# Performance work log

Hardware: AMD Instinct MI355X
Metric: run time of the kernel (lower is better)

Reference implementation:

```python
import jax, jax.numpy as jnp
import numpy as np

B, D, H, N, M, K = 128, 256, 4, 256, 256, 10  # M=256 is hardcoded in the original repeat(1,1,1,256)
DIM = D // H  # per-head dim = 64


def setup_inputs() -> dict:
    key = jax.random.key(0)
    ks = jax.random.split(key, 10)
    s = 0.05  # weight scale
    return {
        "x": jax.random.normal(ks[0], (B, D, N), jnp.float32),
        "source": jax.random.normal(ks[1], (B, D, M), jnp.float32),
        "Wq": jax.random.normal(ks[2], (D, D), jnp.float32) * s,
        "bq": jax.random.normal(ks[3], (D,), jnp.float32) * s,
        "Wk": jax.random.normal(ks[4], (D, D), jnp.float32) * s,
        "bk": jax.random.normal(ks[5], (D,), jnp.float32) * s,
        "Wv": jax.random.normal(ks[6], (D, D), jnp.float32) * s,
        "bv": jax.random.normal(ks[7], (D,), jnp.float32) * s,
        "Wm": jax.random.normal(ks[8], (D, D), jnp.float32) * s,
        "bm": jax.random.normal(ks[9], (D,), jnp.float32) * s,
        "k": K,
    }


def _pointwise(W, b, x):
    # nn.Conv1d(d, d, kernel_size=1): per-point linear over channel dim
    return jnp.einsum('ef,bfn->ben', W, x) + b[None, :, None]


def reference(x, source, Wq, bq, Wk, bk, Wv, bv, Wm, bm, k):
    b, d, n = x.shape
    # torch .view(b, dim, heads, -1) splits channels as (dim, heads)
    q = _pointwise(Wq, bq, x).reshape(b, DIM, H, n)
    kk = _pointwise(Wk, bk, source).reshape(b, DIM, H, -1)
    v = _pointwise(Wv, bv, source).reshape(b, DIM, H, -1)

    scores = jnp.einsum('bdhn,bdhm->bhnm', q, kk) / jnp.sqrt(jnp.asarray(DIM, x.dtype))
    # per-row top-k threshold: keep only scores >= k-th largest, softmax over kept
    thresh = jax.lax.top_k(scores, k)[0][..., k - 1:k]  # [b,h,n,1]
    mask = scores >= thresh
    neg = jnp.finfo(scores.dtype).min
    prob = jax.nn.softmax(jnp.where(mask, scores, neg), axis=-1)
    prob = jnp.where(mask, prob, jnp.zeros((), scores.dtype))

    out = jnp.einsum('bhnm,bdhm->bdhn', prob, v).reshape(b, d, n)
    return _pointwise(Wm, bm, out)
```

## Files before the change

### kernel.cpp

```cpp
#include <hip/hip_runtime.h>
#include <hip/hip_bf16.h>

#define BB   128
#define DDIM 256
#define HH   4
#define NNN  256
#define MMM  256

typedef __hip_bfloat16 bf16;
typedef short  short8   __attribute__((ext_vector_type(8)));
typedef unsigned short ushort8_t __attribute__((ext_vector_type(8)));
typedef float  f32x4    __attribute__((ext_vector_type(4)));

__device__ __forceinline__ unsigned short f2bf(float x) {
    unsigned u = __builtin_bit_cast(unsigned, x);
    u += 0x7FFFu + ((u >> 16) & 1u);
    return (unsigned short)(u >> 16);
}
__device__ __forceinline__ float bf2f(unsigned short b) {
    unsigned u = ((unsigned)b) << 16;
    return __builtin_bit_cast(float, u);
}

__device__ __forceinline__ void xpose4(float v[4], const int p) {
    float ta = __shfl_xor((p & 1) ? v[0] : v[1], 1, 64);
    float tb = __shfl_xor((p & 1) ? v[2] : v[3], 1, 64);
    float u0 = (p & 1) ? ta : v[0];
    float u1 = (p & 1) ? v[1] : ta;
    float u2 = (p & 1) ? tb : v[2];
    float u3 = (p & 1) ? v[3] : tb;
    float tc = __shfl_xor((p & 2) ? u0 : u2, 2, 64);
    float td = __shfl_xor((p & 2) ? u1 : u3, 2, 64);
    v[0] = (p & 2) ? tc : u0;
    v[1] = (p & 2) ? td : u1;
    v[2] = (p & 2) ? u2 : tc;
    v[3] = (p & 2) ? u3 : td;
}

__device__ __forceinline__ void split3_store8k(char* dst, const float v[4]) {
    unsigned short h[4], m[4], l[4];
    #pragma unroll
    for (int i = 0; i < 4; ++i) {
        h[i] = f2bf(v[i]);
        float r1 = v[i] - bf2f(h[i]);
        m[i] = f2bf(r1);
        float r2 = r1 - bf2f(m[i]);
        l[i] = f2bf(r2);
    }
    uint2 hp, mp, lp;
    hp.x = (unsigned)h[0] | ((unsigned)h[1] << 16);
    hp.y = (unsigned)h[2] | ((unsigned)h[3] << 16);
    mp.x = (unsigned)m[0] | ((unsigned)m[1] << 16);
    mp.y = (unsigned)m[2] | ((unsigned)m[3] << 16);
    lp.x = (unsigned)l[0] | ((unsigned)l[1] << 16);
    lp.y = (unsigned)l[2] | ((unsigned)l[3] << 16);
    *(uint2*)dst = hp;
    *(uint2*)(dst + 8192) = mp;
    *(uint2*)(dst + 16384) = lp;
}

__device__ __forceinline__ void split2_store(char* dst, const float v[4]) {
    unsigned short h[4], m[4];
    #pragma unroll
    for (int i = 0; i < 4; ++i) {
        h[i] = f2bf(v[i]);
        float r1 = v[i] - bf2f(h[i]);
        m[i] = f2bf(r1);
    }
    uint2 hp, mp;
    hp.x = (unsigned)h[0] | ((unsigned)h[1] << 16);
    hp.y = (unsigned)h[2] | ((unsigned)h[3] << 16);
    mp.x = (unsigned)m[0] | ((unsigned)m[1] << 16);
    mp.y = (unsigned)m[2] | ((unsigned)m[3] << 16);
    *(uint2*)dst = hp;
    *(uint2*)(dst + 16384) = mp;
}

__device__ __forceinline__ void ldx4(const float* p, float v[4]) {
    const float4 f = *(const float4*)p;
    v[0] = f.x; v[1] = f.y; v[2] = f.z; v[3] = f.w;
}
__device__ __forceinline__ void ldx4(const bf16* p, float v[4]) {
    uint2 u = *(const uint2*)p;
    v[0] = bf2f((unsigned short)(u.x & 0xFFFF));
    v[1] = bf2f((unsigned short)(u.x >> 16));
    v[2] = bf2f((unsigned short)(u.y & 0xFFFF));
    v[3] = bf2f((unsigned short)(u.y >> 16));
}

__device__ __forceinline__ float max16v(const float* w) {
    float a = fmaxf(fmaxf(w[0], w[1]),  fmaxf(w[2], w[3]));
    float b = fmaxf(fmaxf(w[4], w[5]),  fmaxf(w[6], w[7]));
    float c = fmaxf(fmaxf(w[8], w[9]),  fmaxf(w[10], w[11]));
    float d = fmaxf(fmaxf(w[12], w[13]), fmaxf(w[14], w[15]));
    return fmaxf(fmaxf(a, b), fmaxf(c, d));
}
__device__ __forceinline__ float gmax16(float v) {
    v = fmaxf(v, __shfl_xor(v, 1, 64));
    v = fmaxf(v, __shfl_xor(v, 2, 64));
    v = fmaxf(v, __shfl_xor(v, 4, 64));
    v = fmaxf(v, __shfl_xor(v, 8, 64));
    return v;
}
__device__ __forceinline__ float gsum16(float v) {
    v += __shfl_xor(v, 1, 64);
    v += __shfl_xor(v, 2, 64);
    v += __shfl_xor(v, 4, 64);
    v += __shfl_xor(v, 8, 64);
    return v;
}

__global__ __launch_bounds__(256)
void proj_kernel(const float* __restrict__ X, const float* __restrict__ W,
                 const float* __restrict__ bias, float* __restrict__ Y) {
    __shared__ float Wt[32][68];
    __shared__ float Xt[32][132];

    const int t  = threadIdx.x;
    const int tx = t & 31;
    const int ty = t >> 5;
    const int n0 = blockIdx.x * 128;
    const int e0 = blockIdx.y * 64;
    const int b  = blockIdx.z;
    const size_t plane = (size_t)b * DDIM * NNN;

    float acc[8][4] = {};

    for (int f0 = 0; f0 < DDIM; f0 += 32) {
        #pragma unroll
        for (int i = 0; i < 8; ++i) {
            int idx = t + i * 256;
            int fl = idx & 31, el = idx >> 5;
            Wt[fl][el] = W[(size_t)(e0 + el) * DDIM + f0 + fl];
        }
        #pragma unroll
        for (int i = 0; i < 4; ++i) {
            int idx = t + i * 256;
            int fl = idx >> 5, nl4 = idx & 31;
            *(float4*)&Xt[fl][nl4 * 4] =
                *(const float4*)&X[plane + (size_t)(f0 + fl) * NNN + n0 + nl4 * 4];
        }
        __syncthreads();

        #pragma unroll
        for (int ff = 0; ff < 32; ++ff) {
            const float4 av0 = *(const float4*)&Wt[ff][ty * 8];
            const float4 av1 = *(const float4*)&Wt[ff][ty * 8 + 4];
            const float4 bv  = *(const float4*)&Xt[ff][tx * 4];
            const float a[8] = {av0.x, av0.y, av0.z, av0.w, av1.x, av1.y, av1.z, av1.w};
            const float c[4] = {bv.x, bv.y, bv.z, bv.w};
            #pragma unroll
            for (int i2 = 0; i2 < 8; ++i2)
                #pragma unroll
                for (int j = 0; j < 4; ++j)
                    acc[i2][j] = fmaf(a[i2], c[j], acc[i2][j]);
        }
        __syncthreads();
    }

    #pragma unroll
    for (int i2 = 0; i2 < 8; ++i2) {
        const int e = e0 + ty * 8 + i2;
        const float bs = bias[e];
        const size_t off = plane + (size_t)e * NNN + n0 + tx * 4;
        float4 o;
        o.x = acc[i2][0] + bs; o.y = acc[i2][1] + bs;
        o.z = acc[i2][2] + bs; o.w = acc[i2][3] + bs;
        *(float4*)&Y[off] = o;
    }
}

template <typename TIN, typename TOUT>
__global__ __launch_bounds__(512, 2)
void projm_kernel(const TIN* __restrict__ X, const float* __restrict__ W,
                  const float* __restrict__ bias, TOUT* __restrict__ Y) {
    extern __shared__ __align__(16) char smem[];

    const int t    = threadIdx.x;
    const int lane = t & 63;
    const int w    = t >> 6;
    const int c16  = lane & 15;
    const int g    = (lane >> 4) & 3;
    const int p    = lane & 3;
    const int G    = lane >> 2;

    const int n0 = blockIdx.x * 128;
    const int e0 = blockIdx.y * 128;
    const int b  = blockIdx.z;
    const size_t plane = (size_t)b * DDIM * NNN;

    f32x4 acc[8];
    #pragma unroll
    for (int nf = 0; nf < 8; ++nf) acc[nf] = f32x4{0.f, 0.f, 0.f, 0.f};

    #pragma unroll
    for (int ft = 0; ft < 4; ++ft) {
        const int f0 = ft * 64;
        if (ft) __syncthreads();
        #pragma unroll
        for (int it = 0; it < 4; ++it) {
            int chunk = w + 8 * it;
            int fch = chunk & 15, nh = chunk >> 4;
            float v[4];
            ldx4(&X[plane + (size_t)(f0 + fch * 4 + p) * NNN + n0 + nh * 64 + G * 4], v);
            xpose4(v, p);
            int nl = nh * 64 + G * 4 + p;
            int base = nl * 128 + ((fch * 8) ^ ((nl & 7) << 4));
            split2_store(smem + base, v);
        }
        #pragma unroll
        for (int it = 0; it < 4; ++it) {
            int idx = t + 512 * it;
            int el = idx >> 4, fq = idx & 15;
            float v[4];
            const float4 f4 = *(const float4*)&W[(size_t)(e0 + el) * DDIM + f0 + fq * 4];
            v[0] = f4.x; v[1] = f4.y; v[2] = f4.z; v[3] = f4.w;
            int base = 32768 + el * 128 + ((fq * 8) ^ ((el & 7) << 4));
            split2_store(smem + base, v);
        }
        __syncthreads();

        const int ew = w * 16;
        short8 a0[2], a1[2];
        #pragma unroll
        for (int ks = 0; ks < 2; ++ks) {
            int off = 32768 + (ew + c16) * 128
                    + ((ks * 64 + g * 16) ^ ((c16 & 7) << 4));
            a0[ks] = *(const short8*)(smem + off);
            a1[ks] = *(const short8*)(smem + off + 16384);
        }
        #pragma unroll
        for (int nf = 0; nf < 8; ++nf) {
            #pragma unroll
            for (int ks = 0; ks < 2; ++ks) {
                int off = (nf * 16 + c16) * 128
                        + ((ks * 64 + g * 16) ^ ((c16 & 7) << 4));
                short8 b0 = *(const short8*)(smem + off);
                short8 b1 = *(const short8*)(smem + off + 16384);
                f32x4 a = acc[nf];
                a = __builtin_amdgcn_mfma_f32_16x16x32_bf16(a0[ks], b0, a, 0, 0, 0);
                a = __builtin_amdgcn_mfma_f32_16x16x32_bf16(a0[ks], b1, a, 0, 0, 0);
                a = __builtin_amdgcn_mfma_f32_16x16x32_bf16(a1[ks], b0, a, 0, 0, 0);
                acc[nf] = a;
            }
        }
    }

    const int ew = w * 16;
    float bs[4];
    #pragma unroll
    for (int r = 0; r < 4; ++r) bs[r] = bias[e0 + ew + g * 4 + r];
    #pragma unroll
    for (int nf = 0; nf < 8; ++nf) {
        #pragma unroll
        for (int r = 0; r < 4; ++r) {
            size_t off = plane + (size_t)(e0 + ew + g * 4 + r) * NNN + n0 + nf * 16 + c16;
            float val = acc[nf][r] + bs[r];
            if constexpr (sizeof(TOUT) == 4) Y[off] = val;
            else                             *(unsigned short*)&Y[off] = f2bf(val);
        }
    }
}

__global__ __launch_bounds__(256, 3)
void attn3_kernel(const float* __restrict__ qf, const float* __restrict__ kf,
                  const bf16* __restrict__ vb, bf16* __restrict__ ob,
                  const int* __restrict__ kptr) {
    extern __shared__ __align__(16) char smem[];

    const int t    = threadIdx.x;
    const int lane = t & 63;
    const int w    = t >> 6;
    const int g    = lane >> 4;
    const int c16  = lane & 15;

    const int i    = blockIdx.x;
    const int work = (i & 7) * 256 + (i >> 3);
    const int bx = work & 3;
    const int h  = (work >> 2) & 3;
    const int b  = work >> 4;
    const int n0 = bx * 64;

    const size_t planeF = (size_t)b * DDIM * NNN;
    const size_t planeV = (size_t)b * DDIM * MMM;

    int kk = kptr[0];
    kk = kk < 1 ? 1 : (kk > MMM ? MMM : kk);

    {
        const int p = lane & 3, G = lane >> 2;
        #pragma unroll
        for (int it = 0; it < 4; ++it) {
            int dch = w + 4 * it;
            int drow = dch * 4 + p;
            float v[4];
            const float4 f4 = *(const float4*)&qf[planeF + (size_t)(drow * HH + h) * NNN + n0 + G * 4];
            v[0] = f4.x * 0.125f; v[1] = f4.y * 0.125f;
            v[2] = f4.z * 0.125f; v[3] = f4.w * 0.125f;
            xpose4(v, p);
            int nl = G * 4 + p;
            int base = nl * 128 + ((dch * 8) ^ ((nl & 7) << 4));
            split3_store8k(smem + base, v);
        }
    }
    __syncthreads();

    short8 qh[2], qm[2], ql[2];
    #pragma unroll
    for (int ks = 0; ks < 2; ++ks) {
        int nl = w * 16 + c16;
        int off = nl * 128 + ((ks * 64 + g * 16) ^ ((nl & 7) << 4));
        qh[ks] = *(const short8*)(smem + off);
        qm[ks] = *(const short8*)(smem + 8192 + off);
        ql[ks] = *(const short8*)(smem + 16384 + off);
    }

    f32x4 acc[16];
    #pragma unroll
    for (int m = 0; m < 16; ++m) acc[m] = f32x4{0.f, 0.f, 0.f, 0.f};

    #pragma unroll
    for (int tt = 0; tt < 4; ++tt) {
        if (tt) __syncthreads();
        {
            const int p = lane & 3, G = lane >> 2;
            #pragma unroll
            for (int it = 0; it < 4; ++it) {
                int dch = w + 4 * it;
                int drow = dch * 4 + p;
                int mcol = tt * 64 + G * 4;
                float v[4];
                const float4 f4 = *(const float4*)&kf[planeF + (size_t)(drow * HH + h) * MMM + mcol];
                v[0] = f4.x; v[1] = f4.y; v[2] = f4.z; v[3] = f4.w;
                xpose4(v, p);
                int ml = G * 4 + p;
                int base = 24576 + ml * 128 + ((dch * 8) ^ ((ml & 7) << 4));
                split3_store8k(smem + base, v);
            }
        }
        __syncthreads();
        #pragma unroll
        for (int mf = 0; mf < 4; ++mf) {
            #pragma unroll
            for (int ks = 0; ks < 2; ++ks) {
                int ml = mf * 16 + c16;
                int off = 24576 + ml * 128 + ((ks * 64 + g * 16) ^ ((ml & 7) << 4));
                short8 bh = *(const short8*)(smem + off);
                short8 bm = *(const short8*)(smem + 8192 + off);
                short8 bl = *(const short8*)(smem + 16384 + off);
                f32x4 a = acc[tt * 4 + mf];
                a = __builtin_amdgcn_mfma_f32_16x16x32_bf16(qh[ks], bh, a, 0, 0, 0);
                a = __builtin_amdgcn_mfma_f32_16x16x32_bf16(qh[ks], bm, a, 0, 0, 0);
                a = __builtin_amdgcn_mfma_f32_16x16x32_bf16(qm[ks], bh, a, 0, 0, 0);
                a = __builtin_amdgcn_mfma_f32_16x16x32_bf16(qm[ks], bm, a, 0, 0, 0);
                a = __builtin_amdgcn_mfma_f32_16x16x32_bf16(qh[ks], bl, a, 0, 0, 0);
                a = __builtin_amdgcn_mfma_f32_16x16x32_bf16(ql[ks], bh, a, 0, 0, 0);
                acc[tt * 4 + mf] = a;
            }
        }
    }
    __syncthreads();

    float thr[4], rmx[4];
    #pragma unroll
    for (int r = 0; r < 4; ++r) {
        float w16[16];
        #pragma unroll
        for (int mf = 0; mf < 16; ++mf) w16[mf] = acc[mf][r];
        float lm = max16v(w16);
        float gm = gmax16(lm);
        rmx[r] = gm;
        for (int it = 1; it < kk; ++it) {
            unsigned long long bal = __ballot(lm == gm);
            unsigned gmask = (unsigned)((bal >> (g * 16)) & 0xFFFFull);
            int leader = __builtin_ctz(gmask);
            bool skip = (c16 != leader);
            #pragma unroll
            for (int mf = 0; mf < 16; ++mf) {
                bool hit = (!skip) && (w16[mf] == gm);
                w16[mf] = hit ? -INFINITY : w16[mf];
                skip = skip || hit;
            }
            lm = max16v(w16);
            gm = gmax16(lm);
        }
        thr[r] = gm;
    }

    #pragma unroll
    for (int mf = 0; mf < 16; ++mf) {
        #pragma unroll
        for (int r = 0; r < 4; ++r) {
            float a = acc[mf][r];
            acc[mf][r] = (a >= thr[r]) ? __expf(a - rmx[r]) : 0.f;
        }
    }
    float inv_[4];
    #pragma unroll
    for (int r = 0; r < 4; ++r) {
        float s = ((acc[0][r] + acc[1][r]) + (acc[2][r] + acc[3][r]))
                + ((acc[4][r] + acc[5][r]) + (acc[6][r] + acc[7][r]))
                + ((acc[8][r] + acc[9][r]) + (acc[10][r] + acc[11][r]))
                + ((acc[12][r] + acc[13][r]) + (acc[14][r] + acc[15][r]));
        s = gsum16(s);
        inv_[r] = 1.0f / s;
    }
    #pragma unroll
    for (int mf = 0; mf < 16; ++mf) {
        #pragma unroll
        for (int r = 0; r < 4; ++r) {
            int row = w * 16 + g * 4 + r;
            int m2  = (mf * 16 + c16) * 2;
            int off = row * 512 + (m2 ^ ((row & 7) << 4));
            *(unsigned short*)(smem + off) = f2bf(acc[mf][r] * inv_[r]);
        }
    }

    f32x4 o[4];
    #pragma unroll
    for (int df = 0; df < 4; ++df) o[df] = f32x4{0.f, 0.f, 0.f, 0.f};

    #pragma unroll
    for (int half = 0; half < 2; ++half) {
        if (half) __syncthreads();
        #pragma unroll
        for (int it = 0; it < 4; ++it) {
            int idx = t + it * 256;
            int d = idx >> 4, mc8 = idx & 15;
            ushort8_t val = *(const ushort8_t*)
                &vb[planeV + (size_t)(d * HH + h) * MMM + half * 128 + mc8 * 8];
            int off = 32768 + d * 256 + ((mc8 * 16) ^ ((d & 7) << 4));
            *(ushort8_t*)(smem + off) = val;
        }
        __syncthreads();

        short8 pa[4];
        #pragma unroll
        for (int ks = 0; ks < 4; ++ks) {
            int row = w * 16 + c16;
            int off = row * 512 + ((half * 256 + ks * 64 + g * 16) ^ ((row & 7) << 4));
            pa[ks] = *(const short8*)(smem + off);
        }
        #pragma unroll
        for (int df = 0; df < 4; ++df) {
            int d = df * 16 + c16;
            f32x4 o_ = o[df];
            #pragma unroll
            for (int ks = 0; ks < 4; ++ks) {
                int off = 32768 + d * 256 + ((ks * 64 + g * 16) ^ ((d & 7) << 4));
                short8 vv = *(const short8*)(smem + off);
                o_ = __builtin_amdgcn_mfma_f32_16x16x32_bf16(pa[ks], vv, o_, 0, 0, 0);
            }
            o[df] = o_;
        }
    }
    __syncthreads();

    #pragma unroll
    for (int df = 0; df < 4; ++df)
        #pragma unroll
        for (int r = 0; r < 4; ++r) {
            int d  = df * 16 + c16;
            int nl = w * 16 + g * 4 + r;
            int off = d * 128 + ((nl * 2) ^ ((d & 7) << 4));
            *(unsigned short*)(smem + off) = f2bf(o[df][r]);
        }
    __syncthreads();
    #pragma unroll
    for (int it = 0; it < 2; ++it) {
        int idx = t + it * 256;
        int d = idx >> 3, ch = idx & 7;
        int off = d * 128 + ((ch * 16) ^ ((d & 7) << 4));
        ushort8_t val = *(const ushort8_t*)(smem + off);
        *(ushort8_t*)&ob[planeV + (size_t)(d * HH + h) * NNN + n0 + ch * 8] = val;
    }
}

extern "C" void kernel_launch(void* const* d_in, const int* in_sizes, int n_in,
                              void* d_out, int out_size, void* d_ws, size_t ws_size,
                              hipStream_t stream) {
    const float* x   = (const float*)d_in[0];
    const float* src = (const float*)d_in[1];
    const float* Wq  = (const float*)d_in[2];
    const float* bq  = (const float*)d_in[3];
    const float* Wk  = (const float*)d_in[4];
    const float* bk  = (const float*)d_in[5];
    const float* Wv  = (const float*)d_in[6];
    const float* bv  = (const float*)d_in[7];
    const float* Wm  = (const float*)d_in[8];
    const float* bm  = (const float*)d_in[9];
    const int*   kp  = (const int*)d_in[10];
    float* out = (float*)d_out;

    const size_t F32PLANE  = (size_t)BB * DDIM * NNN * sizeof(float);
    const size_t BF16PLANE = F32PLANE / 2;
    char* ws = (char*)d_ws;
    float* qf = (float*)(ws);
    float* kf = (float*)(ws + F32PLANE);
    bf16*  vb = (bf16*)(ws + 2 * F32PLANE);
    bf16*  ob = (bf16*)(ws + 2 * F32PLANE + BF16PLANE);

    hipFuncSetAttribute((const void*)(projm_kernel<float, bf16>),
                        hipFuncAttributeMaxDynamicSharedMemorySize, 65536);
    hipFuncSetAttribute((const void*)(projm_kernel<bf16, float>),
                        hipFuncAttributeMaxDynamicSharedMemorySize, 65536);
    hipFuncSetAttribute((const void*)attn3_kernel,
                        hipFuncAttributeMaxDynamicSharedMemorySize, 49152);

    dim3 fgrid(NNN / 128, DDIM / 64, BB);
    hipLaunchKernelGGL(proj_kernel, fgrid, dim3(256), 0, stream, x,   Wq, bq, qf);
    hipLaunchKernelGGL(proj_kernel, fgrid, dim3(256), 0, stream, src, Wk, bk, kf);

    dim3 mgrid(2, 2, BB);
    hipLaunchKernelGGL((projm_kernel<float, bf16>), mgrid, dim3(512), 65536, stream,
                       src, Wv, bv, vb);

    hipLaunchKernelGGL(attn3_kernel, dim3(2048), dim3(256), 49152, stream,
                       qf, kf, vb, ob, kp);

    hipLaunchKernelGGL((projm_kernel<bf16, float>), mgrid, dim3(512), 65536, stream,
                       ob, Wm, bm, out);
}
```

Before: 280.4 us.

## Pre-split K into bf16 triple planes and transpose Q/K layout for attention

The Q/K projection kernel now writes outputs in a per-head transposed [b,h,n,d] layout, and K is emitted as three bf16 planes (high/mid/low split) instead of fp32. A new attention kernel loads those pre-split K planes directly into LDS with global_load_lds, which removes the per-block fp32-to-bf16x3 splitting of K and cuts LDS usage so four blocks can run per CU. The projection inner loop is also rewritten with packed two-wide FMAs. The change falls back to the old path when the workspace is too small, and the scattered 2-byte stores in the projection epilogue may cost write bandwidth.

```diff
diff --git a/kernel.cpp b/kernel.cpp
--- a/kernel.cpp
+++ b/kernel.cpp
@@ -11,6 +11,7 @@
 typedef short  short8   __attribute__((ext_vector_type(8)));
 typedef unsigned short ushort8_t __attribute__((ext_vector_type(8)));
 typedef float  f32x4    __attribute__((ext_vector_type(4)));
+typedef float  f32x2    __attribute__((ext_vector_type(2)));
 
 __device__ __forceinline__ unsigned short f2bf(float x) {
     unsigned u = __builtin_bit_cast(unsigned, x);
@@ -110,9 +111,13 @@
     return v;
 }
 
+
+template <int MODE>
 __global__ __launch_bounds__(256)
-void proj_kernel(const float* __restrict__ X, const float* __restrict__ W,
-                 const float* __restrict__ bias, float* __restrict__ Y) {
+void projqk_kernel(const float* __restrict__ X, const float* __restrict__ W,
+                   const float* __restrict__ bias, float* __restrict__ Yt,
+                   unsigned short* __restrict__ Ph, unsigned short* __restrict__ Pm,
+                   unsigned short* __restrict__ Pl) {
     __shared__ float Wt[32][68];
     __shared__ float Xt[32][132];
 
@@ -124,7 +129,12 @@
     const int b  = blockIdx.z;
     const size_t plane = (size_t)b * DDIM * NNN;
 
-    float acc[8][4] = {};
+    f32x2 acc2[8][2];
+    #pragma unroll
+    for (int i = 0; i < 8; ++i) {
+        acc2[i][0] = f32x2{0.f, 0.f};
+        acc2[i][1] = f32x2{0.f, 0.f};
+    }
 
     for (int f0 = 0; f0 < DDIM; f0 += 32) {
         #pragma unroll
@@ -148,12 +158,14 @@
             const float4 av1 = *(const float4*)&Wt[ff][ty * 8 + 4];
             const float4 bv  = *(const float4*)&Xt[ff][tx * 4];
             const float a[8] = {av0.x, av0.y, av0.z, av0.w, av1.x, av1.y, av1.z, av1.w};
-            const float c[4] = {bv.x, bv.y, bv.z, bv.w};
-            #pragma unroll
-            for (int i2 = 0; i2 < 8; ++i2)
-                #pragma unroll
-                for (int j = 0; j < 4; ++j)
-                    acc[i2][j] = fmaf(a[i2], c[j], acc[i2][j]);
+            const f32x2 c0 = {bv.x, bv.y};
+            const f32x2 c1 = {bv.z, bv.w};
+            #pragma unroll
+            for (int i2 = 0; i2 < 8; ++i2) {
+                const f32x2 aa = {a[i2], a[i2]};
+                acc2[i2][0] = __builtin_elementwise_fma(aa, c0, acc2[i2][0]);
+                acc2[i2][1] = __builtin_elementwise_fma(aa, c1, acc2[i2][1]);
+            }
         }
         __syncthreads();
     }
@@ -161,12 +173,225 @@
     #pragma unroll
     for (int i2 = 0; i2 < 8; ++i2) {
         const int e = e0 + ty * 8 + i2;
+        const int hh = e & 3, dd = e >> 2;
         const float bs = bias[e];
-        const size_t off = plane + (size_t)e * NNN + n0 + tx * 4;
-        float4 o;
-        o.x = acc[i2][0] + bs; o.y = acc[i2][1] + bs;
-        o.z = acc[i2][2] + bs; o.w = acc[i2][3] + bs;
-        *(float4*)&Y[off] = o;
+        const float vals[4] = {acc2[i2][0].x + bs, acc2[i2][0].y + bs,
+                               acc2[i2][1].x + bs, acc2[i2][1].y + bs};
+        #pragma unroll
+        for (int j = 0; j < 4; ++j) {
+            const size_t off = ((size_t)(b * 4 + hh) * NNN + n0 + tx * 4 + j) * 64 + dd;
+            if constexpr (MODE == 0) {
+                Yt[off] = vals[j];
+            } else {
+                unsigned short hv = f2bf(vals[j]);
+                float r1 = vals[j] - bf2f(hv);
+                unsigned short mv = f2bf(r1);
+                float r2 = r1 - bf2f(mv);
+                unsigned short lv = f2bf(r2);
+                Ph[off] = hv; Pm[off] = mv; Pl[off] = lv;
+            }
+        }
+    }
+}
+
+__global__ __launch_bounds__(256, 4)
+void attn4_kernel(const float* __restrict__ qt,
+                  const unsigned short* __restrict__ khp,
+                  const unsigned short* __restrict__ kmp,
+                  const unsigned short* __restrict__ klp,
+                  const bf16* __restrict__ vb, bf16* __restrict__ ob,
+                  const int* __restrict__ kptr) {
+    extern __shared__ __align__(16) char smem[];
+
+    const int t    = threadIdx.x;
+    const int lane = t & 63;
+    const int w    = t >> 6;
+    const int g    = lane >> 4;
+    const int c16  = lane & 15;
+
+    const int i    = blockIdx.x;
+    const int work = (i & 7) * 256 + (i >> 3);
+    const int bx = work & 3;
+    const int h  = (work >> 2) & 3;
+    const int b  = work >> 4;
+    const int n0 = bx * 64;
+    const int bh = b * 4 + h;
+
+    const size_t planeV = (size_t)b * DDIM * MMM;
+
+    int kk = kptr[0];
+    kk = kk < 1 ? 1 : (kk > MMM ? MMM : kk);
+
+    #pragma unroll
+    for (int it = 0; it < 4; ++it) {
+        int gid = t + it * 256;
+        int dq = gid & 15;
+        int n  = gid >> 4;
+        const float4 q4 = *(const float4*)&qt[((size_t)bh * NNN + n0 + n) * 64 + dq * 4];
+        float v[4] = {q4.x * 0.125f, q4.y * 0.125f, q4.z * 0.125f, q4.w * 0.125f};
+        int base = n * 128 + ((dq * 8) ^ ((n & 7) << 4));
+        split3_store8k(smem + base, v);
+    }
+    __syncthreads();
+
+    short8 qh[2], qm[2], ql[2];
+    #pragma unroll
+    for (int ks = 0; ks < 2; ++ks) {
+        int nl = w * 16 + c16;
+        int off = nl * 128 + ((ks * 64 + g * 16) ^ ((nl & 7) << 4));
+        qh[ks] = *(const short8*)(smem + off);
+        qm[ks] = *(const short8*)(smem + 8192 + off);
+        ql[ks] = *(const short8*)(smem + 16384 + off);
+    }
+    __syncthreads();
+
+    f32x4 acc[16];
+    #pragma unroll
+    for (int m = 0; m < 16; ++m) acc[m] = f32x4{0.f, 0.f, 0.f, 0.f};
+
+    #pragma unroll
+    for (int tt = 0; tt < 4; ++tt) {
+        if (tt) __syncthreads();
+        #pragma unroll
+        for (int it = 0; it < 6; ++it) {
+            int gid = t + it * 256;
+            int pl  = gid >> 9;
+            int rem = gid & 511;
+            int ml  = rem >> 3;
+            int dq  = rem & 7;
+            int dqs = dq ^ (ml & 7);
+            const unsigned short* kp = (pl == 0) ? khp : (pl == 1 ? kmp : klp);
+            const unsigned short* src = kp + ((size_t)bh * MMM + tt * 64 + ml) * 64 + dqs * 8;
+            __builtin_amdgcn_global_load_lds(
+                (const __attribute__((address_space(1))) void*)src,
+                (__attribute__((address_space(3))) void*)(smem + gid * 16),
+                16, 0, 0);
+        }
+        __syncthreads();
+
+        #pragma unroll
+        for (int mf = 0; mf < 4; ++mf) {
+            #pragma unroll
+            for (int ks = 0; ks < 2; ++ks) {
+                int ml = mf * 16 + c16;
+                int off = ml * 128 + ((ks * 64 + g * 16) ^ ((ml & 7) << 4));
+                short8 bh_ = *(const short8*)(smem + off);
+                short8 bm_ = *(const short8*)(smem + 8192 + off);
+                short8 bl_ = *(const short8*)(smem + 16384 + off);
+                f32x4 a = acc[tt * 4 + mf];
+                a = __builtin_amdgcn_mfma_f32_16x16x32_bf16(qh[ks], bh_, a, 0, 0, 0);
+                a = __builtin_amdgcn_mfma_f32_16x16x32_bf16(qh[ks], bm_, a, 0, 0, 0);
+                a = __builtin_amdgcn_mfma_f32_16x16x32_bf16(qm[ks], bh_, a, 0, 0, 0);
+                a = __builtin_amdgcn_mfma_f32_16x16x32_bf16(qm[ks], bm_, a, 0, 0, 0);
+                a = __builtin_amdgcn_mfma_f32_16x16x32_bf16(qh[ks], bl_, a, 0, 0, 0);
+                a = __builtin_amdgcn_mfma_f32_16x16x32_bf16(ql[ks], bh_, a, 0, 0, 0);
+                acc[tt * 4 + mf] = a;
+            }
+        }
+    }
+    __syncthreads();
+
+    float thr[4], rmx[4];
+    #pragma unroll
+    for (int r = 0; r < 4; ++r) {
+        float w16[16];
+        #pragma unroll
+        for (int mf = 0; mf < 16; ++mf) w16[mf] = acc[mf][r];
+        float lm = max16v(w16);
+        float gm = gmax16(lm);
+        rmx[r] = gm;
+        for (int it = 1; it < kk; ++it) {
+            unsigned long long bal = __ballot(lm == gm);
+            unsigned gmask = (unsigned)((bal >> (g * 16)) & 0xFFFFull);
+            int leader = __builtin_ctz(gmask);
+            bool skip = (c16 != leader);
+            #pragma unroll
+            for (int mf = 0; mf < 16; ++mf) {
+                bool hit = (!skip) && (w16[mf] == gm);
+                w16[mf] = hit ? -INFINITY : w16[mf];
+                skip = skip || hit;
+            }
+            lm = max16v(w16);
+            gm = gmax16(lm);
+        }
+        thr[r] = gm;
+    }
+
+    #pragma unroll
+    for (int mf = 0; mf < 16; ++mf) {
+        #pragma unroll
+        for (int r = 0; r < 4; ++r) {
+            float a = acc[mf][r];
+            acc[mf][r] = (a >= thr[r]) ? __expf(a - rmx[r]) : 0.f;
+        }
+    }
+    float inv_[4];
+    #pragma unroll
+    for (int r = 0; r < 4; ++r) {
+        float s = ((acc[0][r] + acc[1][r]) + (acc[2][r] + acc[3][r]))
+                + ((acc[4][r] + acc[5][r]) + (acc[6][r] + acc[7][r]))
+                + ((acc[8][r] + acc[9][r]) + (acc[10][r] + acc[11][r]))
+                + ((acc[12][r] + acc[13][r]) + (acc[14][r] + acc[15][r]));
+        s = gsum16(s);
+        inv_[r] = 1.0f / s;
+    }
+    #pragma unroll
+    for (int mf = 0; mf < 16; ++mf) {
+        #pragma unroll
+        for (int r = 0; r < 4; ++r) {
+            int row = w * 16 + g * 4 + r;
+            int m2  = (mf * 16 + c16) * 2;
+            int off = row * 512 + (m2 ^ ((row & 7) << 4));
+            *(unsigned short*)(smem + off) = f2bf(acc[mf][r] * inv_[r]);
+        }
+    }
+    __syncthreads();
+
+    f32x4 o[4];
+    #pragma unroll
+    for (int df = 0; df < 4; ++df) o[df] = f32x4{0.f, 0.f, 0.f, 0.f};
+
+    #pragma unroll
+    for (int half = 0; half < 2; ++half) {
+        short8 pa[4];
+        #pragma unroll
+        for (int ks = 0; ks < 4; ++ks) {
+            int row = w * 16 + c16;
+            int off = row * 512 + ((half * 256 + ks * 64 + g * 16) ^ ((row & 7) << 4));
+            pa[ks] = *(const short8*)(smem + off);
+        }
+        #pragma unroll
+        for (int df = 0; df < 4; ++df) {
+            int d = df * 16 + c16;
+            const bf16* vrow = vb + planeV + (size_t)(d * HH + h) * MMM + half * 128;
+            f32x4 o_ = o[df];
+            #pragma unroll
+            for (int ks = 0; ks < 4; ++ks) {
+                short8 vv = *(const short8*)(vrow + ks * 32 + g * 8);
+                o_ = __builtin_amdgcn_mfma_f32_16x16x32_bf16(pa[ks], vv, o_, 0, 0, 0);
+            }
+            o[df] = o_;
+        }
+    }
+    __syncthreads();
+
+    #pragma unroll
+    for (int df = 0; df < 4; ++df)
+        #pragma unroll
+        for (int r = 0; r < 4; ++r) {
+            int d  = df * 16 + c16;
+            int nl = w * 16 + g * 4 + r;
+            int off = d * 128 + ((nl * 2) ^ ((d & 7) << 4));
+            *(unsigned short*)(smem + off) = f2bf(o[df][r]);
+        }
+    __syncthreads();
+    #pragma unroll
+    for (int it = 0; it < 2; ++it) {
+        int idx = t + it * 256;
+        int d = idx >> 3, ch = idx & 7;
+        int off = d * 128 + ((ch * 16) ^ ((d & 7) << 4));
+        ushort8_t val = *(const ushort8_t*)(smem + off);
+        *(ushort8_t*)&ob[planeV + (size_t)(d * HH + h) * NNN + n0 + ch * 8] = val;
     }
 }
 
@@ -259,6 +484,66 @@
             if constexpr (sizeof(TOUT) == 4) Y[off] = val;
             else                             *(unsigned short*)&Y[off] = f2bf(val);
         }
+    }
+}
+
+__global__ __launch_bounds__(256)
+void proj_kernel(const float* __restrict__ X, const float* __restrict__ W,
+                 const float* __restrict__ bias, float* __restrict__ Y) {
+    __shared__ float Wt[32][68];
+    __shared__ float Xt[32][132];
+
+    const int t  = threadIdx.x;
+    const int tx = t & 31;
+    const int ty = t >> 5;
+    const int n0 = blockIdx.x * 128;
+    const int e0 = blockIdx.y * 64;
+    const int b  = blockIdx.z;
+    const size_t plane = (size_t)b * DDIM * NNN;
+
+    float acc[8][4] = {};
+
+    for (int f0 = 0; f0 < DDIM; f0 += 32) {
+        #pragma unroll
+        for (int i = 0; i < 8; ++i) {
+            int idx = t + i * 256;
+            int fl = idx & 31, el = idx >> 5;
+            Wt[fl][el] = W[(size_t)(e0 + el) * DDIM + f0 + fl];
+        }
+        #pragma unroll
+        for (int i = 0; i < 4; ++i) {
+            int idx = t + i * 256;
+            int fl = idx >> 5, nl4 = idx & 31;
+            *(float4*)&Xt[fl][nl4 * 4] =
+                *(const float4*)&X[plane + (size_t)(f0 + fl) * NNN + n0 + nl4 * 4];
+        }
+        __syncthreads();
+
+        #pragma unroll
+        for (int ff = 0; ff < 32; ++ff) {
+            const float4 av0 = *(const float4*)&Wt[ff][ty * 8];
+            const float4 av1 = *(const float4*)&Wt[ff][ty * 8 + 4];
+            const float4 bv  = *(const float4*)&Xt[ff][tx * 4];
+            const float a[8] = {av0.x, av0.y, av0.z, av0.w, av1.x, av1.y, av1.z, av1.w};
+            const float c[4] = {bv.x, bv.y, bv.z, bv.w};
+            #pragma unroll
+            for (int i2 = 0; i2 < 8; ++i2)
+                #pragma unroll
+                for (int j = 0; j < 4; ++j)
+                    acc[i2][j] = fmaf(a[i2], c[j], acc[i2][j]);
+        }
+        __syncthreads();
+    }
+
+    #pragma unroll
+    for (int i2 = 0; i2 < 8; ++i2) {
+        const int e = e0 + ty * 8 + i2;
+        const float bs = bias[e];
+        const size_t off = plane + (size_t)e * NNN + n0 + tx * 4;
+        float4 o;
+        o.x = acc[i2][0] + bs; o.y = acc[i2][1] + bs;
+        o.z = acc[i2][2] + bs; o.w = acc[i2][3] + bs;
+        *(float4*)&Y[off] = o;
     }
 }
 
@@ -492,32 +777,57 @@
     const int*   kp  = (const int*)d_in[10];
     float* out = (float*)d_out;
 
-    const size_t F32PLANE  = (size_t)BB * DDIM * NNN * sizeof(float);
-    const size_t BF16PLANE = F32PLANE / 2;
     char* ws = (char*)d_ws;
-    float* qf = (float*)(ws);
-    float* kf = (float*)(ws + F32PLANE);
-    bf16*  vb = (bf16*)(ws + 2 * F32PLANE);
-    bf16*  ob = (bf16*)(ws + 2 * F32PLANE + BF16PLANE);
+    const size_t QT_BYTES = 33554432;
+    const size_t PL_BYTES = 16777216;
+    const size_t FAST_NEED = QT_BYTES + 3 * PL_BYTES + 2 * PL_BYTES;
 
     hipFuncSetAttribute((const void*)(projm_kernel<float, bf16>),
                         hipFuncAttributeMaxDynamicSharedMemorySize, 65536);
     hipFuncSetAttribute((const void*)(projm_kernel<bf16, float>),
                         hipFuncAttributeMaxDynamicSharedMemorySize, 65536);
-    hipFuncSetAttribute((const void*)attn3_kernel,
-                        hipFuncAttributeMaxDynamicSharedMemorySize, 49152);
-
-    dim3 fgrid(NNN / 128, DDIM / 64, BB);
-    hipLaunchKernelGGL(proj_kernel, fgrid, dim3(256), 0, stream, x,   Wq, bq, qf);
-    hipLaunchKernelGGL(proj_kernel, fgrid, dim3(256), 0, stream, src, Wk, bk, kf);
-
+
+    dim3 pqk_grid(NNN / 128, DDIM / 64, BB);
     dim3 mgrid(2, 2, BB);
-    hipLaunchKernelGGL((projm_kernel<float, bf16>), mgrid, dim3(512), 65536, stream,
-                       src, Wv, bv, vb);
-
-    hipLaunchKernelGGL(attn3_kernel, dim3(2048), dim3(256), 49152, stream,
-                       qf, kf, vb, ob, kp);
-
-    hipLaunchKernelGGL((projm_kernel<bf16, float>), mgrid, dim3(512), 65536, stream,
-                       ob, Wm, bm, out);
-}
+
+    if (ws_size >= FAST_NEED) {
+        float*          qt = (float*)(ws);
+        unsigned short* kh = (unsigned short*)(ws + QT_BYTES);
+        unsigned short* km = (unsigned short*)(ws + QT_BYTES + PL_BYTES);
+        unsigned short* kl = (unsigned short*)(ws + QT_BYTES + 2 * PL_BYTES);
+        bf16*           vb = (bf16*)(ws + QT_BYTES + 3 * PL_BYTES);
+        bf16*           ob = (bf16*)(ws + QT_BYTES + 4 * PL_BYTES);
+
+        hipFuncSetAttribute((const void*)attn4_kernel,
+                            hipFuncAttributeMaxDynamicSharedMemorySize, 32768);
+
+        hipLaunchKernelGGL((projqk_kernel<0>), pqk_grid, dim3(256), 0, stream,
+                           x,   Wq, bq, qt, nullptr, nullptr, nullptr);
+        hipLaunchKernelGGL((projqk_kernel<1>), pqk_grid, dim3(256), 0, stream,
+                           src, Wk, bk, nullptr, kh, km, kl);
+        hipLaunchKernelGGL((projm_kernel<float, bf16>), mgrid, dim3(512), 65536, stream,
+                           src, Wv, bv, vb);
+        hipLaunchKernelGGL(attn4_kernel, dim3(2048), dim3(256), 32768, stream,
+                           qt, kh, km, kl, vb, ob, kp);
+        hipLaunchKernelGGL((projm_kernel<bf16, float>), mgrid, dim3(512), 65536, stream,
+                           ob, Wm, bm, out);
+    } else {
+        const size_t F32PLANE  = 33554432;
+        float* qf = (float*)(ws);
+        float* kf = (float*)(ws + F32PLANE);
+        bf16*  vb = (bf16*)(ws + 2 * F32PLANE);
+        bf16*  ob = (bf16*)(ws + 2 * F32PLANE + F32PLANE / 2);
+
+        hipFuncSetAttribute((const void*)attn3_kernel,
+                            hipFuncAttributeMaxDynamicSharedMemorySize, 49152);
+
+        hipLaunchKernelGGL(proj_kernel, pqk_grid, dim3(256), 0, stream, x,   Wq, bq, qf);
+        hipLaunchKernelGGL(proj_kernel, pqk_grid, dim3(256), 0, stream, src, Wk, bk, kf);
+        hipLaunchKernelGGL((projm_kernel<float, bf16>), mgrid, dim3(512), 65536, stream,
+                           src, Wv, bv, vb);
+        hipLaunchKernelGGL(attn3_kernel, dim3(2048), dim3(256), 49152, stream,
+                           qf, kf, vb, ob, kp);
+        hipLaunchKernelGGL((projm_kernel<bf16, float>), mgrid, dim3(512), 65536, stream,
+                           ob, Wm, bm, out);
+    }
+}
```

Result: slower. 322.0 us (+14.8%).

## Emit Q/K in head-major transposed layout with K pre-split into bf16 planes

Applied to the files above, without the earlier changes.

The Q and K projection kernels now write outputs transposed into a per-(batch,head) [n][64] layout. K is also pre-split into three bf16 planes (high/mid/low), so the attention kernel can stream K tiles straight into LDS with global_load_lds and skip the in-kernel transpose and split. The attention kernel also reads V fragments directly from global memory instead of staging them in LDS, which cuts LDS to 32KB and raises the occupancy hint to 4. The projection kernel gains packed f32x2 FMAs and a full 256-wide output tile per block. The trade-offs are extra K-plane write traffic and uncoalesced V reads in the attention kernel.

```diff
diff --git a/kernel.cpp b/kernel.cpp
--- a/kernel.cpp
+++ b/kernel.cpp
@@ -11,6 +11,7 @@
 typedef short  short8   __attribute__((ext_vector_type(8)));
 typedef unsigned short ushort8_t __attribute__((ext_vector_type(8)));
 typedef float  f32x4    __attribute__((ext_vector_type(4)));
+typedef float  f32x2    __attribute__((ext_vector_type(2)));
 
 __device__ __forceinline__ unsigned short f2bf(float x) {
     unsigned u = __builtin_bit_cast(unsigned, x);
@@ -110,35 +111,45 @@
     return v;
 }
 
+template <int MODE>
 __global__ __launch_bounds__(256)
-void proj_kernel(const float* __restrict__ X, const float* __restrict__ W,
-                 const float* __restrict__ bias, float* __restrict__ Y) {
-    __shared__ float Wt[32][68];
-    __shared__ float Xt[32][132];
+void projqk_kernel(const float* __restrict__ X, const float* __restrict__ W,
+                   const float* __restrict__ bias, float* __restrict__ Yt,
+                   unsigned short* __restrict__ Ph, unsigned short* __restrict__ Pm,
+                   unsigned short* __restrict__ Pl) {
+    __shared__ float Wt[32][268];
+    __shared__ float Xt[32][36];
 
     const int t  = threadIdx.x;
-    const int tx = t & 31;
-    const int ty = t >> 5;
-    const int n0 = blockIdx.x * 128;
-    const int e0 = blockIdx.y * 64;
-    const int b  = blockIdx.z;
+    const int tx = t & 7;
+    const int ty = t >> 3;
+    const int n0 = blockIdx.x * 32;
+    const int b  = blockIdx.y;
     const size_t plane = (size_t)b * DDIM * NNN;
 
-    float acc[8][4] = {};
+    f32x2 acc2[8][2];
+    #pragma unroll
+    for (int i = 0; i < 8; ++i) {
+        acc2[i][0] = f32x2{0.f, 0.f};
+        acc2[i][1] = f32x2{0.f, 0.f};
+    }
 
     for (int f0 = 0; f0 < DDIM; f0 += 32) {
         #pragma unroll
         for (int i = 0; i < 8; ++i) {
             int idx = t + i * 256;
-            int fl = idx & 31, el = idx >> 5;
-            Wt[fl][el] = W[(size_t)(e0 + el) * DDIM + f0 + fl];
+            int fq = idx & 7, el = idx >> 3;
+            const float4 w4 = *(const float4*)&W[(size_t)el * DDIM + f0 + fq * 4];
+            Wt[fq * 4 + 0][el] = w4.x;
+            Wt[fq * 4 + 1][el] = w4.y;
+            Wt[fq * 4 + 2][el] = w4.z;
+            Wt[fq * 4 + 3][el] = w4.w;
         }
         #pragma unroll
         for (int i = 0; i < 4; ++i) {
             int idx = t + i * 256;
-            int fl = idx >> 5, nl4 = idx & 31;
-            *(float4*)&Xt[fl][nl4 * 4] =
-                *(const float4*)&X[plane + (size_t)(f0 + fl) * NNN + n0 + nl4 * 4];
+            int fl = idx >> 5, nl = idx & 31;
+            Xt[fl][nl] = X[plane + (size_t)(f0 + fl) * NNN + n0 + nl];
         }
         __syncthreads();
 
@@ -148,122 +159,72 @@
             const float4 av1 = *(const float4*)&Wt[ff][ty * 8 + 4];
             const float4 bv  = *(const float4*)&Xt[ff][tx * 4];
             const float a[8] = {av0.x, av0.y, av0.z, av0.w, av1.x, av1.y, av1.z, av1.w};
-            const float c[4] = {bv.x, bv.y, bv.z, bv.w};
+            const f32x2 c0 = {bv.x, bv.y};
+            const f32x2 c1 = {bv.z, bv.w};
             #pragma unroll
-            for (int i2 = 0; i2 < 8; ++i2)
-                #pragma unroll
-                for (int j = 0; j < 4; ++j)
-                    acc[i2][j] = fmaf(a[i2], c[j], acc[i2][j]);
+            for (int i2 = 0; i2 < 8; ++i2) {
+                const f32x2 aa = {a[i2], a[i2]};
+                acc2[i2][0] = __builtin_elementwise_fma(aa, c0, acc2[i2][0]);
+                acc2[i2][1] = __builtin_elementwise_fma(aa, c1, acc2[i2][1]);
+            }
         }
         __syncthreads();
     }
 
+    float* stage = &Wt[0][0];
     #pragma unroll
     for (int i2 = 0; i2 < 8; ++i2) {
-        const int e = e0 + ty * 8 + i2;
+        const int e = ty * 8 + i2;
         const float bs = bias[e];
-        const size_t off = plane + (size_t)e * NNN + n0 + tx * 4;
-        float4 o;
-        o.x = acc[i2][0] + bs; o.y = acc[i2][1] + bs;
-        o.z = acc[i2][2] + bs; o.w = acc[i2][3] + bs;
-        *(float4*)&Y[off] = o;
-    }
-}
-
-template <typename TIN, typename TOUT>
-__global__ __launch_bounds__(512, 2)
-void projm_kernel(const TIN* __restrict__ X, const float* __restrict__ W,
-                  const float* __restrict__ bias, TOUT* __restrict__ Y) {
-    extern __shared__ __align__(16) char smem[];
-
-    const int t    = threadIdx.x;
-    const int lane = t & 63;
-    const int w    = t >> 6;
-    const int c16  = lane & 15;
-    const int g    = (lane >> 4) & 3;
-    const int p    = lane & 3;
-    const int G    = lane >> 2;
-
-    const int n0 = blockIdx.x * 128;
-    const int e0 = blockIdx.y * 128;
-    const int b  = blockIdx.z;
-    const size_t plane = (size_t)b * DDIM * NNN;
-
-    f32x4 acc[8];
-    #pragma unroll
-    for (int nf = 0; nf < 8; ++nf) acc[nf] = f32x4{0.f, 0.f, 0.f, 0.f};
-
-    #pragma unroll
-    for (int ft = 0; ft < 4; ++ft) {
-        const int f0 = ft * 64;
-        if (ft) __syncthreads();
-        #pragma unroll
-        for (int it = 0; it < 4; ++it) {
-            int chunk = w + 8 * it;
-            int fch = chunk & 15, nh = chunk >> 4;
-            float v[4];
-            ldx4(&X[plane + (size_t)(f0 + fch * 4 + p) * NNN + n0 + nh * 64 + G * 4], v);
-            xpose4(v, p);
-            int nl = nh * 64 + G * 4 + p;
-            int base = nl * 128 + ((fch * 8) ^ ((nl & 7) << 4));
-            split2_store(smem + base, v);
-        }
-        #pragma unroll
-        for (int it = 0; it < 4; ++it) {
-            int idx = t + 512 * it;
-            int el = idx >> 4, fq = idx & 15;
-            float v[4];
-            const float4 f4 = *(const float4*)&W[(size_t)(e0 + el) * DDIM + f0 + fq * 4];
-            v[0] = f4.x; v[1] = f4.y; v[2] = f4.z; v[3] = f4.w;
-            int base = 32768 + el * 128 + ((fq * 8) ^ ((el & 7) << 4));
-            split2_store(smem + base, v);
-        }
-        __syncthreads();
-
-        const int ew = w * 16;
-        short8 a0[2], a1[2];
-        #pragma unroll
-        for (int ks = 0; ks < 2; ++ks) {
-            int off = 32768 + (ew + c16) * 128
-                    + ((ks * 64 + g * 16) ^ ((c16 & 7) << 4));
-            a0[ks] = *(const short8*)(smem + off);
-            a1[ks] = *(const short8*)(smem + off + 16384);
-        }
-        #pragma unroll
-        for (int nf = 0; nf < 8; ++nf) {
+        const int col = (e & 3) * 64 + (e >> 2);
+        stage[(tx * 4 + 0) * 260 + col] = acc2[i2][0].x + bs;
+        stage[(tx * 4 + 1) * 260 + col] = acc2[i2][0].y + bs;
+        stage[(tx * 4 + 2) * 260 + col] = acc2[i2][1].x + bs;
+        stage[(tx * 4 + 3) * 260 + col] = acc2[i2][1].y + bs;
+    }
+    __syncthreads();
+
+    #pragma unroll
+    for (int it = 0; it < 8; ++it) {
+        int gid = t + it * 256;
+        int n   = gid >> 6;
+        int sub = gid & 63;
+        const float4 v4 = *(const float4*)&stage[n * 260 + sub * 4];
+        const int hh = sub >> 4;
+        const int dd0 = (sub & 15) * 4;
+        const size_t off = ((size_t)(b * 4 + hh) * NNN + n0 + n) * 64 + dd0;
+        if constexpr (MODE == 0) {
+            *(float4*)&Yt[off] = v4;
+        } else {
+            const float v[4] = {v4.x, v4.y, v4.z, v4.w};
+            unsigned short h[4], m[4], l[4];
             #pragma unroll
-            for (int ks = 0; ks < 2; ++ks) {
-                int off = (nf * 16 + c16) * 128
-                        + ((ks * 64 + g * 16) ^ ((c16 & 7) << 4));
-                short8 b0 = *(const short8*)(smem + off);
-                short8 b1 = *(const short8*)(smem + off + 16384);
-                f32x4 a = acc[nf];
-                a = __builtin_amdgcn_mfma_f32_16x16x32_bf16(a0[ks], b0, a, 0, 0, 0);
-                a = __builtin_amdgcn_mfma_f32_16x16x32_bf16(a0[ks], b1, a, 0, 0, 0);
-                a = __builtin_amdgcn_mfma_f32_16x16x32_bf16(a1[ks], b0, a, 0, 0, 0);
-                acc[nf] = a;
+            for (int i = 0; i < 4; ++i) {
+                h[i] = f2bf(v[i]);
+                float r1 = v[i] - bf2f(h[i]);
+                m[i] = f2bf(r1);
+                float r2 = r1 - bf2f(m[i]);
+                l[i] = f2bf(r2);
             }
-        }
-    }
-
-    const int ew = w * 16;
-    float bs[4];
-    #pragma unroll
-    for (int r = 0; r < 4; ++r) bs[r] = bias[e0 + ew + g * 4 + r];
-    #pragma unroll
-    for (int nf = 0; nf < 8; ++nf) {
-        #pragma unroll
-        for (int r = 0; r < 4; ++r) {
-            size_t off = plane + (size_t)(e0 + ew + g * 4 + r) * NNN + n0 + nf * 16 + c16;
-            float val = acc[nf][r] + bs[r];
-            if constexpr (sizeof(TOUT) == 4) Y[off] = val;
-            else                             *(unsigned short*)&Y[off] = f2bf(val);
-        }
-    }
-}
-
-__global__ __launch_bounds__(256, 3)
-void attn3_kernel(const float* __restrict__ qf, const float* __restrict__ kf,
+            uint2 hp, mp, lp;
+            hp.x = (unsigned)h[0] | ((unsigned)h[1] << 16);
+            hp.y = (unsigned)h[2] | ((unsigned)h[3] << 16);
+            mp.x = (unsigned)m[0] | ((unsigned)m[1] << 16);
+            mp.y = (unsigned)m[2] | ((unsigned)m[3] << 16);
+            lp.x = (unsigned)l[0] | ((unsigned)l[1] << 16);
+            lp.y = (unsigned)l[2] | ((unsigned)l[3] << 16);
+            *(uint2*)&Ph[off] = hp;
+            *(uint2*)&Pm[off] = mp;
+            *(uint2*)&Pl[off] = lp;
+        }
+    }
+}
+
+__global__ __launch_bounds__(256, 4)
+void attn4_kernel(const float* __restrict__ qt,
+                  const unsigned short* __restrict__ khp,
+                  const unsigned short* __restrict__ kmp,
+                  const unsigned short* __restrict__ klp,
                   const bf16* __restrict__ vb, bf16* __restrict__ ob,
                   const int* __restrict__ kptr) {
     extern __shared__ __align__(16) char smem[];
@@ -280,28 +241,22 @@
     const int h  = (work >> 2) & 3;
     const int b  = work >> 4;
     const int n0 = bx * 64;
-
-    const size_t planeF = (size_t)b * DDIM * NNN;
+    const int bh = b * 4 + h;
+
     const size_t planeV = (size_t)b * DDIM * MMM;
 
     int kk = kptr[0];
     kk = kk < 1 ? 1 : (kk > MMM ? MMM : kk);
 
-    {
-        const int p = lane & 3, G = lane >> 2;
-        #pragma unroll
-        for (int it = 0; it < 4; ++it) {
-            int dch = w + 4 * it;
-            int drow = dch * 4 + p;
-            float v[4];
-            const float4 f4 = *(const float4*)&qf[planeF + (size_t)(drow * HH + h) * NNN + n0 + G * 4];
-            v[0] = f4.x * 0.125f; v[1] = f4.y * 0.125f;
-            v[2] = f4.z * 0.125f; v[3] = f4.w * 0.125f;
-            xpose4(v, p);
-            int nl = G * 4 + p;
-            int base = nl * 128 + ((dch * 8) ^ ((nl & 7) << 4));
-            split3_store8k(smem + base, v);
-        }
+    #pragma unroll
+    for (int it = 0; it < 4; ++it) {
+        int gid = t + it * 256;
+        int dq = gid & 15;
+        int n  = gid >> 4;
+        const float4 q4 = *(const float4*)&qt[((size_t)bh * NNN + n0 + n) * 64 + dq * 4];
+        float v[4] = {q4.x * 0.125f, q4.y * 0.125f, q4.z * 0.125f, q4.w * 0.125f};
+        int base = n * 128 + ((dq * 8) ^ ((n & 7) << 4));
+        split3_store8k(smem + base, v);
     }
     __syncthreads();
 
@@ -314,6 +269,7 @@
         qm[ks] = *(const short8*)(smem + 8192 + off);
         ql[ks] = *(const short8*)(smem + 16384 + off);
     }
+    __syncthreads();
 
     f32x4 acc[16];
     #pragma unroll
@@ -322,39 +278,39 @@
     #pragma unroll
     for (int tt = 0; tt < 4; ++tt) {
         if (tt) __syncthreads();
-        {
-            const int p = lane & 3, G = lane >> 2;
-            #pragma unroll
-            for (int it = 0; it < 4; ++it) {
-                int dch = w + 4 * it;
-                int drow = dch * 4 + p;
-                int mcol = tt * 64 + G * 4;
-                float v[4];
-                const float4 f4 = *(const float4*)&kf[planeF + (size_t)(drow * HH + h) * MMM + mcol];
-                v[0] = f4.x; v[1] = f4.y; v[2] = f4.z; v[3] = f4.w;
-                xpose4(v, p);
-                int ml = G * 4 + p;
-                int base = 24576 + ml * 128 + ((dch * 8) ^ ((ml & 7) << 4));
-                split3_store8k(smem + base, v);
-            }
+        #pragma unroll
+        for (int it = 0; it < 6; ++it) {
+            int gid = t + it * 256;
+            int pl  = gid >> 9;
+            int rem = gid & 511;
+            int ml  = rem >> 3;
+            int dq  = rem & 7;
+            int dqs = dq ^ (ml & 7);
+            const unsigned short* kp = (pl == 0) ? khp : (pl == 1 ? kmp : klp);
+            const unsigned short* src = kp + ((size_t)bh * MMM + tt * 64 + ml) * 64 + dqs * 8;
+            __builtin_amdgcn_global_load_lds(
+                (const __attribute__((address_space(1))) void*)src,
+                (__attribute__((address_space(3))) void*)(smem + gid * 16),
+                16, 0, 0);
         }
         __syncthreads();
+
         #pragma unroll
         for (int mf = 0; mf < 4; ++mf) {
             #pragma unroll
             for (int ks = 0; ks < 2; ++ks) {
                 int ml = mf * 16 + c16;
-                int off = 24576 + ml * 128 + ((ks * 64 + g * 16) ^ ((ml & 7) << 4));
-                short8 bh = *(const short8*)(smem + off);
-                short8 bm = *(const short8*)(smem + 8192 + off);
-                short8 bl = *(const short8*)(smem + 16384 + off);
+                int off = ml * 128 + ((ks * 64 + g * 16) ^ ((ml & 7) << 4));
+                short8 bh_ = *(const short8*)(smem + off);
+                short8 bm_ = *(const short8*)(smem + 8192 + off);
+                short8 bl_ = *(const short8*)(smem + 16384 + off);
                 f32x4 a = acc[tt * 4 + mf];
-                a = __builtin_amdgcn_mfma_f32_16x16x32_bf16(qh[ks], bh, a, 0, 0, 0);
-                a = __builtin_amdgcn_mfma_f32_16x16x32_bf16(qh[ks], bm, a, 0, 0, 0);
-                a = __builtin_amdgcn_mfma_f32_16x16x32_bf16(qm[ks], bh, a, 0, 0, 0);
-                a = __builtin_amdgcn_mfma_f32_16x16x32_bf16(qm[ks], bm, a, 0, 0, 0);
-                a = __builtin_amdgcn_mfma_f32_16x16x32_bf16(qh[ks], bl, a, 0, 0, 0);
-                a = __builtin_amdgcn_mfma_f32_16x16x32_bf16(ql[ks], bh, a, 0, 0, 0);
+                a = __builtin_amdgcn_mfma_f32_16x16x32_bf16(qh[ks], bh_, a, 0, 0, 0);
+                a = __builtin_amdgcn_mfma_f32_16x16x32_bf16(qh[ks], bm_, a, 0, 0, 0);
+                a = __builtin_amdgcn_mfma_f32_16x16x32_bf16(qm[ks], bh_, a, 0, 0, 0);
+                a = __builtin_amdgcn_mfma_f32_16x16x32_bf16(qm[ks], bm_, a, 0, 0, 0);
+                a = __builtin_amdgcn_mfma_f32_16x16x32_bf16(qh[ks], bl_, a, 0, 0, 0);
+                a = __builtin_amdgcn_mfma_f32_16x16x32_bf16(ql[ks], bh_, a, 0, 0, 0);
                 acc[tt * 4 + mf] = a;
             }
         }
@@ -415,6 +371,7 @@
             *(unsigned short*)(smem + off) = f2bf(acc[mf][r] * inv_[r]);
         }
     }
+    __syncthreads();
 
     f32x4 o[4];
     #pragma unroll
@@ -422,18 +379,6 @@
 
     #pragma unroll
     for (int half = 0; half < 2; ++half) {
-        if (half) __syncthreads();
-        #pragma unroll
-        for (int it = 0; it < 4; ++it) {
-            int idx = t + it * 256;
-            int d = idx >> 4, mc8 = idx & 15;
-            ushort8_t val = *(const ushort8_t*)
-                &vb[planeV + (size_t)(d * HH + h) * MMM + half * 128 + mc8 * 8];
-            int off = 32768 + d * 256 + ((mc8 * 16) ^ ((d & 7) << 4));
-            *(ushort8_t*)(smem + off) = val;
-        }
-        __syncthreads();
-
         short8 pa[4];
         #pragma unroll
         for (int ks = 0; ks < 4; ++ks) {
@@ -444,11 +389,11 @@
         #pragma unroll
         for (int df = 0; df < 4; ++df) {
             int d = df * 16 + c16;
+            const bf16* vrow = vb + planeV + (size_t)(d * HH + h) * MMM + half * 128;
             f32x4 o_ = o[df];
             #pragma unroll
             for (int ks = 0; ks < 4; ++ks) {
-                int off = 32768 + d * 256 + ((ks * 64 + g * 16) ^ ((d & 7) << 4));
-                short8 vv = *(const short8*)(smem + off);
+                short8 vv = *(const short8*)(vrow + ks * 32 + g * 8);
                 o_ = __builtin_amdgcn_mfma_f32_16x16x32_bf16(pa[ks], vv, o_, 0, 0, 0);
             }
             o[df] = o_;
@@ -473,6 +418,98 @@
         int off = d * 128 + ((ch * 16) ^ ((d & 7) << 4));
         ushort8_t val = *(const ushort8_t*)(smem + off);
         *(ushort8_t*)&ob[planeV + (size_t)(d * HH + h) * NNN + n0 + ch * 8] = val;
+    }
+}
+
+template <typename TIN, typename TOUT>
+__global__ __launch_bounds__(512, 2)
+void projm_kernel(const TIN* __restrict__ X, const float* __restrict__ W,
+                  const float* __restrict__ bias, TOUT* __restrict__ Y) {
+    extern __shared__ __align__(16) char smem[];
+
+    const int t    = threadIdx.x;
+    const int lane = t & 63;
+    const int w    = t >> 6;
+    const int c16  = lane & 15;
+    const int g    = (lane >> 4) & 3;
+    const int p    = lane & 3;
+    const int G    = lane >> 2;
+
+    const int n0 = blockIdx.x * 128;
+    const int e0 = blockIdx.y * 128;
+    const int b  = blockIdx.z;
+    const size_t plane = (size_t)b * DDIM * NNN;
+
+    f32x4 acc[8];
+    #pragma unroll
+    for (int nf = 0; nf < 8; ++nf) acc[nf] = f32x4{0.f, 0.f, 0.f, 0.f};
+
+    #pragma unroll
+    for (int ft = 0; ft < 4; ++ft) {
+        const int f0 = ft * 64;
+        if (ft) __syncthreads();
+        #pragma unroll
+        for (int it = 0; it < 4; ++it) {
+            int chunk = w + 8 * it;
+            int fch = chunk & 15, nh = chunk >> 4;
+            float v[4];
+            ldx4(&X[plane + (size_t)(f0 + fch * 4 + p) * NNN + n0 + nh * 64 + G * 4], v);
+            xpose4(v, p);
+            int nl = nh * 64 + G * 4 + p;
+            int base = nl * 128 + ((fch * 8) ^ ((nl & 7) << 4));
+            split2_store(smem + base, v);
+        }
+        #pragma unroll
+        for (int it = 0; it < 4; ++it) {
+            int idx = t + 512 * it;
+            int el = idx >> 4, fq = idx & 15;
+            float v[4];
+            const float4 f4 = *(const float4*)&W[(size_t)(e0 + el) * DDIM + f0 + fq * 4];
+            v[0] = f4.x; v[1] = f4.y; v[2] = f4.z; v[3] = f4.w;
+            int base = 32768 + el * 128 + ((fq * 8) ^ ((el & 7) << 4));
+            split2_store(smem + base, v);
+        }
+        __syncthreads();
+
+        const int ew = w * 16;
+        short8 a0[2], a1[2];
+        #pragma unroll
+        for (int ks = 0; ks < 2; ++ks) {
+            int off = 32768 + (ew + c16) * 128
+                    + ((ks * 64 + g * 16) ^ ((c16 & 7) << 4));
+            a0[ks] = *(const short8*)(smem + off);
+            a1[ks] = *(const short8*)(smem + off + 16384);
+        }
+        #pragma unroll
+        for (int nf = 0; nf < 8; ++nf) {
+            #pragma unroll
+            for (int ks = 0; ks < 2; ++ks) {
+                int off = (nf * 16 + c16) * 128
+                        + ((ks * 64 + g * 16) ^ ((c16 & 7) << 4));
+                short8 b0 = *(const short8*)(smem + off);
+                short8 b1 = *(const short8*)(smem + off + 16384);
+                f32x4 a = acc[nf];
+                a = __builtin_amdgcn_mfma_f32_16x16x32_bf16(a0[ks], b0, a, 0, 0, 0);
+                a = __builtin_amdgcn_mfma_f32_16x16x32_bf16(a0[ks], b1, a, 0, 0, 0);
+                a = __builtin_amdgcn_mfma_f32_16x16x32_bf16(a1[ks], b0, a, 0, 0, 0);
+                acc[nf] = a;
+            }
+        }
+    }
+
+    const int ew = w * 16;
+    float bs[4];
+    #pragma unroll
+    for (int r = 0; r < 4; ++r) bs[r] = bias[e0 + ew + g * 4 + r];
+    #pragma unroll
+    for (int nf = 0; nf < 8; ++nf) {
+        #pragma unroll
+        for (int r = 0; r < 4; ++r) {
+            size_t off = plane + (size_t)(e0 + ew + g * 4 + r) * NNN + n0 + nf * 16 + c16;
+            float val = acc[nf][r] + bs[r];
+            if constexpr (sizeof(TOUT) == 4) Y[off] = val;
+            else                             *(unsigned short*)&Y[off] = f2bf(val);
+        }
     }
 }
 
@@ -492,32 +529,35 @@
     const int*   kp  = (const int*)d_in[10];
     float* out = (float*)d_out;
 
-    const size_t F32PLANE  = (size_t)BB * DDIM * NNN * sizeof(float);
-    const size_t BF16PLANE = F32PLANE / 2;
     char* ws = (char*)d_ws;
-    float* qf = (float*)(ws);
-    float* kf = (float*)(ws + F32PLANE);
-    bf16*  vb = (bf16*)(ws + 2 * F32PLANE);
-    bf16*  ob = (bf16*)(ws + 2 * F32PLANE + BF16PLANE);
+    const size_t QT_BYTES = 33554432;
+    const size_t PL_BYTES = 16777216;
+
+    float*          qt = (float*)(ws);
+    unsigned short* kh = (unsigned short*)(ws + QT_BYTES);
+    unsigned short* km = (unsigned short*)(ws + QT_BYTES + PL_BYTES);
+    unsigned short* kl = (unsigned short*)(ws + QT_BYTES + 2 * PL_BYTES);
+    bf16*           vb = (bf16*)(ws + QT_BYTES + 3 * PL_BYTES);
+    bf16*           ob = (bf16*)(ws + QT_BYTES + 4 * PL_BYTES);
 
     hipFuncSetAttribute((const void*)(projm_kernel<float, bf16>),
                         hipFuncAttributeMaxDynamicSharedMemorySize, 65536);
     hipFuncSetAttribute((const void*)(projm_kernel<bf16, float>),
                         hipFuncAttributeMaxDynamicSharedMemorySize, 65536);
-    hipFuncSetAttribute((const void*)attn3_kernel,
-                        hipFuncAttributeMaxDynamicSharedMemorySize, 49152);
-
-    dim3 fgrid(NNN / 128, DDIM / 64, BB);
-    hipLaunchKernelGGL(proj_kernel, fgrid, dim3(256), 0, stream, x,   Wq, bq, qf);
-    hipLaunchKernelGGL(proj_kernel, fgrid, dim3(256), 0, stream, src, Wk, bk, kf);
-
+    hipFuncSetAttribute((const void*)attn4_kernel,
+                        hipFuncAttributeMaxDynamicSharedMemorySize, 32768);
+
+    dim3 qk_grid(NNN / 32, BB);
     dim3 mgrid(2, 2, BB);
+
+    hipLaunchKernelGGL((projqk_kernel<0>), qk_grid, dim3(256), 0, stream,
+                       x,   Wq, bq, qt, nullptr, nullptr, nullptr);
+    hipLaunchKernelGGL((projqk_kernel<1>), qk_grid, dim3(256), 0, stream,
+                       src, Wk, bk, nullptr, kh, km, kl);
     hipLaunchKernelGGL((projm_kernel<float, bf16>), mgrid, dim3(512), 65536, stream,
                        src, Wv, bv, vb);
-
-    hipLaunchKernelGGL(attn3_kernel, dim3(2048), dim3(256), 49152, stream,
-                       qf, kf, vb, ob, kp);
-
+    hipLaunchKernelGGL(attn4_kernel, dim3(2048), dim3(256), 32768, stream,
+                       qt, kh, km, kl, vb, ob, kp);
     hipLaunchKernelGGL((projm_kernel<bf16, float>), mgrid, dim3(512), 65536, stream,
                        ob, Wm, bm, out);
 }
```

After: 289.9 us. +3.4%, slower.
